# Kernel optimization log

Measured on AMD Instinct MI355X. Metric: run time of the kernel, lower is better.

The kernel has to match this reference:

```python
import jax, jax.numpy as jnp
import numpy as np

CHANNELS = 1024
T_LEN = 16384
WINDOW = 16
W_MIN, W_MAX = -1.0, 3.0
BETA = 0.95       # snn.Leaky(beta=0.95)
THRESHOLD = 1.0   # snn.Leaky(threshold=1)


def setup_inputs() -> dict:
    key = jax.random.key(0)
    inp = jax.random.normal(key, (CHANNELS, T_LEN), dtype=jnp.float32)
    return {"inp": inp}


def reference(inp):
    C, T = inp.shape
    pad = WINDOW // 2
    inp_padded = jnp.pad(inp, ((0, 0), (pad, pad)))  # [C, T + WINDOW]
    n_steps = T - WINDOW

    def step(carry, t):
        w, mem = carry
        # B: sliding window [C, WINDOW] starting at column t of padded input
        B = jax.lax.dynamic_slice(inp_padded, (0, t), (C, WINDOW))
        # mean(B @ B.T, axis=1) == B @ mean(B, axis=0)  -- avoids [C, C] intermediate
        B_ram = B @ jnp.mean(B, axis=0)
        w = jnp.clip(0.5 * w + 0.5 * B_ram, W_MIN, W_MAX)
        x = B[:, 0]  # == inp_padded[:, t]
        # snntorch Leaky, reset_mechanism='subtract':
        # reset from incoming mem, then mem = beta*mem + input - reset*thr, spk = mem > thr
        reset = (mem > THRESHOLD).astype(inp.dtype)
        mem = BETA * mem + w * x - reset * THRESHOLD
        spk = (mem > THRESHOLD).astype(inp.dtype)
        return (w, mem), spk

    w0 = jnp.ones((C,), dtype=inp.dtype)
    mem0 = jnp.zeros((C,), dtype=inp.dtype)
    _, spks = jax.lax.scan(step, (w0, mem0), jnp.arange(n_steps))  # spks: [n_steps, C]
    # out = deepcopy(inp); out[:, t] = spk for t < T - WINDOW
    out = inp.at[:, :n_steps].set(spks.T)
    return out
```

## Files before the change

### kernel.cpp

```cpp
#include <hip/hip_runtime.h>

#define C_CH   1024
#define T_DIM  16384
#define NSTEPS (T_DIM - 16)
#define PAD    8
#define TP     (T_DIM + 16)
#define CHUNK  256
#define NCHUNK 64
#define WARM   256

#define WS_CM_OFFSET (8u * T_DIM * sizeof(double))

__global__ void colsum_partial(const float* __restrict__ inp, double* __restrict__ part) {
    int col4 = (blockIdx.x * 256 + threadIdx.x) * 4;
    int rc   = blockIdx.y;
    const float* p = inp + (size_t)rc * 128 * T_DIM + col4;
    double ax = 0.0, ay = 0.0, az = 0.0, aw = 0.0;
    #pragma unroll 4
    for (int r = 0; r < 128; ++r) {
        float4 v = *(const float4*)(p + (size_t)r * T_DIM);
        ax += (double)v.x; ay += (double)v.y; az += (double)v.z; aw += (double)v.w;
    }
    double* q = part + (size_t)rc * T_DIM + col4;
    q[0] = ax; q[1] = ay; q[2] = az; q[3] = aw;
}

__global__ void colmean_tail(const double* __restrict__ part, const float* __restrict__ inp,
                             float* __restrict__ cm, float* __restrict__ out) {
    int i = blockIdx.x * 256 + threadIdx.x;
    if (i < TP) {
        float v = 0.0f;
        if (i >= PAD && i < T_DIM + PAD) {
            int col = i - PAD;
            double t = 0.0;
            #pragma unroll
            for (int r = 0; r < 8; ++r) t += part[(size_t)r * T_DIM + col];
            v = (float)(t * (1.0 / 1024.0));
        }
        cm[i] = v;
    }
    if (i < C_CH * 16) {
        int c = i >> 4, j = i & 15;
        size_t idx = (size_t)c * T_DIM + NSTEPS + j;
        out[idx] = inp[idx];
    }
}

__global__ __launch_bounds__(64) void scan_kernel(const float* __restrict__ inp,
                                                  const float* __restrict__ cm,
                                                  float* __restrict__ out) {
    const int k  = blockIdx.x;
    const int c  = blockIdx.y * 64 + threadIdx.x;
    const int t0 = k * CHUNK;
    const int tend = min(t0 + CHUNK, NSTEPS);
    const int tw = (k == 0) ? 0 : t0 - WARM;

    const float* row  = inp + (size_t)c * T_DIM;
    float*       orow = out + (size_t)c * T_DIM;

    float xs[16], ms[16];
    float win = 0.0f;
    #pragma unroll
    for (int j = 0; j < 16; ++j) {
        int s = tw + j;
        float x = (s >= PAD) ? row[s - PAD] : 0.0f;
        float m = cm[s];
        xs[j] = x; ms[j] = m;
        win = fmaf(x, m, win);
    }

    float w = 1.0f, mem = 0.0f;

    float4 a0 = *(const float4*)(row + tw + 8);
    float4 a1 = *(const float4*)(row + tw + 12);
    float4 a2 = *(const float4*)(row + tw + 16);
    float4 a3 = *(const float4*)(row + tw + 20);
    float4 b0 = *(const float4*)(cm + tw + 16);
    float4 b1 = *(const float4*)(cm + tw + 20);
    float4 b2 = *(const float4*)(cm + tw + 24);
    float4 b3 = *(const float4*)(cm + tw + 28);

    for (int t = tw; t < tend; t += 16) {
        float xn[16] = {a0.x,a0.y,a0.z,a0.w, a1.x,a1.y,a1.z,a1.w,
                        a2.x,a2.y,a2.z,a2.w, a3.x,a3.y,a3.z,a3.w};
        float mn[16] = {b0.x,b0.y,b0.z,b0.w, b1.x,b1.y,b1.z,b1.w,
                        b2.x,b2.y,b2.z,b2.w, b3.x,b3.y,b3.z,b3.w};

        int ts = (t + 16 < tend) ? (t + 16) : t;
        a0 = *(const float4*)(row + ts + 8);
        a1 = *(const float4*)(row + ts + 12);
        a2 = *(const float4*)(row + ts + 16);
        a3 = *(const float4*)(row + ts + 20);
        b0 = *(const float4*)(cm + ts + 16);
        b1 = *(const float4*)(cm + ts + 20);
        b2 = *(const float4*)(cm + ts + 24);
        b3 = *(const float4*)(cm + ts + 28);

        float spk[16];
        #pragma unroll
        for (int j = 0; j < 16; ++j) {
            w = fminf(fmaxf(fmaf(0.5f, w, 0.5f * win), -1.0f), 3.0f);
            float x = xs[j];
            float r = (mem > 1.0f) ? 1.0f : 0.0f;
            mem = fmaf(0.95f, mem, fmaf(w, x, -r));
            spk[j] = (mem > 1.0f) ? 1.0f : 0.0f;
            win = fmaf(xn[j], mn[j], fmaf(-x, ms[j], win));
            xs[j] = xn[j]; ms[j] = mn[j];
        }

        if (t >= t0) {
            *(float4*)(orow + t)      = make_float4(spk[0],  spk[1],  spk[2],  spk[3]);
            *(float4*)(orow + t + 4)  = make_float4(spk[4],  spk[5],  spk[6],  spk[7]);
            *(float4*)(orow + t + 8)  = make_float4(spk[8],  spk[9],  spk[10], spk[11]);
            *(float4*)(orow + t + 12) = make_float4(spk[12], spk[13], spk[14], spk[15]);
        }
    }
}

extern "C" void kernel_launch(void* const* d_in, const int* in_sizes, int n_in,
                              void* d_out, int out_size, void* d_ws, size_t ws_size,
                              hipStream_t stream) {
    const float* inp = (const float*)d_in[0];
    float* out = (float*)d_out;
    double* part = (double*)d_ws;
    float* cm = (float*)((char*)d_ws + WS_CM_OFFSET);

    colsum_partial<<<dim3(T_DIM / 1024, 8), 256, 0, stream>>>(inp, part);
    colmean_tail<<<dim3(65), 256, 0, stream>>>(part, inp, cm, out);
    scan_kernel<<<dim3(NCHUNK, C_CH / 64), 64, 0, stream>>>(inp, cm, out);
}
```

Measured before the change: 158.5 us.

## Stage scan input tiles via async global-to-LDS loads with swizzle and double buffering

The scan kernel now loads 64x64 input tiles cooperatively into double-buffered, XOR-swizzled shared memory using global_load_lds. This replaces per-thread strided row loads, which were uncoalesced across channels, and paces them with explicit vmcnt waits. It also remaps the block index to interleave chunks, writes spikes with nontemporal stores, and reshapes colsum_partial to 64-thread blocks with deeper unrolling. The cost is added complexity, hand-written waitcnt assumptions that could break ordering, and LDS use that may reduce occupancy.

```diff
diff --git a/kernel.cpp b/kernel.cpp
--- a/kernel.cpp
+++ b/kernel.cpp
@@ -8,15 +8,19 @@
 #define CHUNK  256
 #define NCHUNK 64
 #define WARM   256
+#define TILE   64
+
+typedef float vf4 __attribute__((ext_vector_type(4)));
 
 #define WS_CM_OFFSET (8u * T_DIM * sizeof(double))
 
-__global__ void colsum_partial(const float* __restrict__ inp, double* __restrict__ part) {
-    int col4 = (blockIdx.x * 256 + threadIdx.x) * 4;
+__global__ __launch_bounds__(64) void colsum_partial(const float* __restrict__ inp,
+                                                     double* __restrict__ part) {
+    int col4 = (blockIdx.x * 64 + threadIdx.x) * 4;
     int rc   = blockIdx.y;
     const float* p = inp + (size_t)rc * 128 * T_DIM + col4;
     double ax = 0.0, ay = 0.0, az = 0.0, aw = 0.0;
-    #pragma unroll 4
+    #pragma unroll 16
     for (int r = 0; r < 128; ++r) {
         float4 v = *(const float4*)(p + (size_t)r * T_DIM);
         ax += (double)v.x; ay += (double)v.y; az += (double)v.z; aw += (double)v.w;
@@ -46,55 +50,107 @@
     }
 }
 
+__device__ __forceinline__ void stage_tile(const float* __restrict__ inp, int ch0,
+                                           int col0, float* dst, int lane) {
+    const int sub = lane >> 4;
+    const int ci  = lane & 15;
+    #pragma unroll
+    for (int ii = 0; ii < 16; ++ii) {
+        int r   = 4 * ii + sub;
+        int q   = ci ^ (r & 7);
+        int col = col0 + q * 4;
+        col = min(max(col, 0), T_DIM - 4);
+        const float* src = inp + (size_t)(ch0 + r) * T_DIM + col;
+        __builtin_amdgcn_global_load_lds(
+            (const __attribute__((address_space(1))) void*)src,
+            (__attribute__((address_space(3))) void*)(dst + ii * 256),
+            16, 0, 0);
+    }
+}
+
 __global__ __launch_bounds__(64) void scan_kernel(const float* __restrict__ inp,
                                                   const float* __restrict__ cm,
                                                   float* __restrict__ out) {
-    const int k  = blockIdx.x;
-    const int c  = blockIdx.y * 64 + threadIdx.x;
-    const int t0 = k * CHUNK;
+    __shared__ float lds[2][64][TILE];
+
+    const int id   = blockIdx.x;
+    const int k    = ((id & 7) << 3) | ((id >> 3) & 7);
+    const int ygrp = id >> 6;
+    const int lane = threadIdx.x;
+    const int ch0  = ygrp * 64;
+    const int c    = ch0 + lane;
+    const int sw   = lane & 7;
+
+    const int t0   = k * CHUNK;
     const int tend = min(t0 + CHUNK, NSTEPS);
-    const int tw = (k == 0) ? 0 : t0 - WARM;
+    const int tw   = (k == 0) ? 0 : t0 - WARM;
+    const int base = tw - PAD;
+    const int span = tend - tw + 16;
+    const int ntiles = (span + TILE - 1) / TILE;
 
-    const float* row  = inp + (size_t)c * T_DIM;
-    float*       orow = out + (size_t)c * T_DIM;
+    float* orow = out + (size_t)c * T_DIM;
+
+    stage_tile(inp, ch0, base,        &lds[0][0][0], lane);
+    stage_tile(inp, ch0, base + TILE, &lds[1][0][0], lane);
+    asm volatile("s_waitcnt vmcnt(16)" ::: "memory");
 
     float xs[16], ms[16];
+    {
+        const float4* lrow0 = (const float4*)&lds[0][lane][0];
+        float4 i0 = lrow0[0 ^ sw];
+        float4 i1 = lrow0[1 ^ sw];
+        float4 i2 = lrow0[2 ^ sw];
+        float4 i3 = lrow0[3 ^ sw];
+        float tmp[16] = {i0.x,i0.y,i0.z,i0.w, i1.x,i1.y,i1.z,i1.w,
+                         i2.x,i2.y,i2.z,i2.w, i3.x,i3.y,i3.z,i3.w};
+        float4 m0 = *(const float4*)(cm + tw);
+        float4 m1 = *(const float4*)(cm + tw + 4);
+        float4 m2 = *(const float4*)(cm + tw + 8);
+        float4 m3 = *(const float4*)(cm + tw + 12);
+        float mt[16] = {m0.x,m0.y,m0.z,m0.w, m1.x,m1.y,m1.z,m1.w,
+                        m2.x,m2.y,m2.z,m2.w, m3.x,m3.y,m3.z,m3.w};
+        #pragma unroll
+        for (int j = 0; j < 16; ++j) {
+            xs[j] = (base + j < 0) ? 0.0f : tmp[j];
+            ms[j] = mt[j];
+        }
+    }
     float win = 0.0f;
     #pragma unroll
-    for (int j = 0; j < 16; ++j) {
-        int s = tw + j;
-        float x = (s >= PAD) ? row[s - PAD] : 0.0f;
-        float m = cm[s];
-        xs[j] = x; ms[j] = m;
-        win = fmaf(x, m, win);
-    }
+    for (int j = 0; j < 16; ++j) win = fmaf(xs[j], ms[j], win);
 
     float w = 1.0f, mem = 0.0f;
 
-    float4 a0 = *(const float4*)(row + tw + 8);
-    float4 a1 = *(const float4*)(row + tw + 12);
-    float4 a2 = *(const float4*)(row + tw + 16);
-    float4 a3 = *(const float4*)(row + tw + 20);
-    float4 b0 = *(const float4*)(cm + tw + 16);
-    float4 b1 = *(const float4*)(cm + tw + 20);
-    float4 b2 = *(const float4*)(cm + tw + 24);
-    float4 b3 = *(const float4*)(cm + tw + 28);
+    const int niter = (tend - tw) >> 4;
+    for (int i = 0; i < niter; ++i) {
+        const int t   = tw + (i << 4);
+        const int nxt = i + 1;
 
-    for (int t = tw; t < tend; t += 16) {
+        if ((nxt & 3) == 0) {
+            const int tn = nxt >> 2;
+            if (tn + 1 < ntiles) {
+                stage_tile(inp, ch0, base + (tn + 1) * TILE, &lds[(tn + 1) & 1][0][0], lane);
+                asm volatile("s_waitcnt vmcnt(16)" ::: "memory");
+            } else {
+                asm volatile("s_waitcnt vmcnt(0)" ::: "memory");
+            }
+        }
+
+        const float4* lrow = (const float4*)&lds[(nxt >> 2) & 1][lane][0];
+        const int qk = (nxt & 3) * 4;
+        float4 a0 = lrow[(qk + 0) ^ sw];
+        float4 a1 = lrow[(qk + 1) ^ sw];
+        float4 a2 = lrow[(qk + 2) ^ sw];
+        float4 a3 = lrow[(qk + 3) ^ sw];
+        float4 b0 = *(const float4*)(cm + t + 16);
+        float4 b1 = *(const float4*)(cm + t + 20);
+        float4 b2 = *(const float4*)(cm + t + 24);
+        float4 b3 = *(const float4*)(cm + t + 28);
+
         float xn[16] = {a0.x,a0.y,a0.z,a0.w, a1.x,a1.y,a1.z,a1.w,
                         a2.x,a2.y,a2.z,a2.w, a3.x,a3.y,a3.z,a3.w};
         float mn[16] = {b0.x,b0.y,b0.z,b0.w, b1.x,b1.y,b1.z,b1.w,
                         b2.x,b2.y,b2.z,b2.w, b3.x,b3.y,b3.z,b3.w};
-
-        int ts = (t + 16 < tend) ? (t + 16) : t;
-        a0 = *(const float4*)(row + ts + 8);
-        a1 = *(const float4*)(row + ts + 12);
-        a2 = *(const float4*)(row + ts + 16);
-        a3 = *(const float4*)(row + ts + 20);
-        b0 = *(const float4*)(cm + ts + 16);
-        b1 = *(const float4*)(cm + ts + 20);
-        b2 = *(const float4*)(cm + ts + 24);
-        b3 = *(const float4*)(cm + ts + 28);
 
         float spk[16];
         #pragma unroll
@@ -109,10 +165,14 @@
         }
 
         if (t >= t0) {
-            *(float4*)(orow + t)      = make_float4(spk[0],  spk[1],  spk[2],  spk[3]);
-            *(float4*)(orow + t + 4)  = make_float4(spk[4],  spk[5],  spk[6],  spk[7]);
-            *(float4*)(orow + t + 8)  = make_float4(spk[8],  spk[9],  spk[10], spk[11]);
-            *(float4*)(orow + t + 12) = make_float4(spk[12], spk[13], spk[14], spk[15]);
+            vf4 s0 = {spk[0],  spk[1],  spk[2],  spk[3]};
+            vf4 s1 = {spk[4],  spk[5],  spk[6],  spk[7]};
+            vf4 s2 = {spk[8],  spk[9],  spk[10], spk[11]};
+            vf4 s3 = {spk[12], spk[13], spk[14], spk[15]};
+            __builtin_nontemporal_store(s0, (vf4*)(orow + t));
+            __builtin_nontemporal_store(s1, (vf4*)(orow + t + 4));
+            __builtin_nontemporal_store(s2, (vf4*)(orow + t + 8));
+            __builtin_nontemporal_store(s3, (vf4*)(orow + t + 12));
         }
     }
 }
@@ -125,7 +185,7 @@
     double* part = (double*)d_ws;
     float* cm = (float*)((char*)d_ws + WS_CM_OFFSET);
 
-    colsum_partial<<<dim3(T_DIM / 1024, 8), 256, 0, stream>>>(inp, part);
+    colsum_partial<<<dim3(64, 8), 64, 0, stream>>>(inp, part);
     colmean_tail<<<dim3(65), 256, 0, stream>>>(part, inp, cm, out);
-    scan_kernel<<<dim3(NCHUNK, C_CH / 64), 64, 0, stream>>>(inp, cm, out);
+    scan_kernel<<<dim3(NCHUNK * (C_CH / 64)), 64, 0, stream>>>(inp, cm, out);
 }
```

New measurement: 255.5 us. 1.61x slower.

## Scan one channel per block with row staged in LDS and bitmask-coalesced output

Applied to the files above, without the earlier changes.

The scan kernel now gives each 64-lane block a single channel. The whole row is loaded into LDS through swizzled global_load_lds, and each lane handles a 256-step segment after warming up over the previous segment. Spikes are packed into bitmasks, exchanged through shared memory and written back as coalesced float4 stores, instead of each thread writing strided rows. The column-sum kernel also changes to 64-thread blocks with a deeper unroll. The block now uses about 64KB of LDS, which limits occupancy. The warmup still duplicates work, now at a fixed 256 steps per segment.

```diff
diff --git a/kernel.cpp b/kernel.cpp
--- a/kernel.cpp
+++ b/kernel.cpp
@@ -1,22 +1,22 @@
 #include <hip/hip_runtime.h>
+#include <stdint.h>
 
 #define C_CH   1024
 #define T_DIM  16384
 #define NSTEPS (T_DIM - 16)
 #define PAD    8
 #define TP     (T_DIM + 16)
-#define CHUNK  256
-#define NCHUNK 64
-#define WARM   256
+#define SEG    256
 
 #define WS_CM_OFFSET (8u * T_DIM * sizeof(double))
 
-__global__ void colsum_partial(const float* __restrict__ inp, double* __restrict__ part) {
-    int col4 = (blockIdx.x * 256 + threadIdx.x) * 4;
+__global__ __launch_bounds__(64) void colsum_partial(const float* __restrict__ inp,
+                                                     double* __restrict__ part) {
+    int col4 = (blockIdx.x * 64 + threadIdx.x) * 4;
     int rc   = blockIdx.y;
     const float* p = inp + (size_t)rc * 128 * T_DIM + col4;
     double ax = 0.0, ay = 0.0, az = 0.0, aw = 0.0;
-    #pragma unroll 4
+    #pragma unroll 32
     for (int r = 0; r < 128; ++r) {
         float4 v = *(const float4*)(p + (size_t)r * T_DIM);
         ax += (double)v.x; ay += (double)v.y; az += (double)v.z; aw += (double)v.w;
@@ -46,74 +46,130 @@
     }
 }
 
+__device__ __forceinline__ float4 swz_ld(const float* base, int b) {
+    int a = (b & ~1023) | ((((b >> 4) & 63) ^ ((b >> 10) & 7)) << 4);
+    return *(const float4*)((const char*)base + a);
+}
+
 __global__ __launch_bounds__(64) void scan_kernel(const float* __restrict__ inp,
                                                   const float* __restrict__ cm,
                                                   float* __restrict__ out) {
-    const int k  = blockIdx.x;
-    const int c  = blockIdx.y * 64 + threadIdx.x;
-    const int t0 = k * CHUNK;
-    const int tend = min(t0 + CHUNK, NSTEPS);
-    const int tw = (k == 0) ? 0 : t0 - WARM;
+    __shared__ float    rowl[T_DIM + 8];
+    __shared__ uint32_t bm[64][8];
 
-    const float* row  = inp + (size_t)c * T_DIM;
-    float*       orow = out + (size_t)c * T_DIM;
+    const int ch   = blockIdx.x;
+    const int lane = threadIdx.x;
+    const float* row  = inp + (size_t)ch * T_DIM;
+    float*       orow = out + (size_t)ch * T_DIM;
+
+    #pragma unroll
+    for (int i = 0; i < 64; ++i) {
+        const float* src = row + i * SEG + ((lane ^ (i & 7)) << 2);
+        __builtin_amdgcn_global_load_lds(
+            (const __attribute__((address_space(1))) void*)src,
+            (__attribute__((address_space(3))) void*)(rowl + i * SEG),
+            16, 0, 0);
+    }
+    if (lane < 2) {
+        *(float4*)(rowl + T_DIM + lane * 4) = make_float4(0.f, 0.f, 0.f, 0.f);
+    }
+    asm volatile("s_waitcnt vmcnt(0)" ::: "memory");
+    __builtin_amdgcn_sched_barrier(0);
+
+    const int sW = (lane == 0) ? 0 : (lane - 1) * SEG;
+    const int sM = lane * SEG;
 
     float xs[16], ms[16];
+    {
+        const float4* cp = (const float4*)(cm + sW);
+        float4 m0 = cp[0], m1 = cp[1], m2 = cp[2], m3 = cp[3];
+        float mt[16] = {m0.x,m0.y,m0.z,m0.w, m1.x,m1.y,m1.z,m1.w,
+                        m2.x,m2.y,m2.z,m2.w, m3.x,m3.y,m3.z,m3.w};
+        #pragma unroll
+        for (int j = 0; j < 16; ++j) ms[j] = mt[j];
+
+        if (sW == 0) {
+            float4 x2 = swz_ld(rowl, 0);
+            float4 x3 = swz_ld(rowl, 16);
+            float xt[8] = {x2.x,x2.y,x2.z,x2.w, x3.x,x3.y,x3.z,x3.w};
+            #pragma unroll
+            for (int j = 0; j < 8; ++j) { xs[j] = 0.0f; xs[j + 8] = xt[j]; }
+        } else {
+            const int b = sW * 4 - 32;
+            float4 x0 = swz_ld(rowl, b),      x1 = swz_ld(rowl, b + 16),
+                   x2 = swz_ld(rowl, b + 32), x3 = swz_ld(rowl, b + 48);
+            float xt[16] = {x0.x,x0.y,x0.z,x0.w, x1.x,x1.y,x1.z,x1.w,
+                            x2.x,x2.y,x2.z,x2.w, x3.x,x3.y,x3.z,x3.w};
+            #pragma unroll
+            for (int j = 0; j < 16; ++j) xs[j] = xt[j];
+        }
+    }
     float win = 0.0f;
     #pragma unroll
-    for (int j = 0; j < 16; ++j) {
-        int s = tw + j;
-        float x = (s >= PAD) ? row[s - PAD] : 0.0f;
-        float m = cm[s];
-        xs[j] = x; ms[j] = m;
-        win = fmaf(x, m, win);
+    for (int j = 0; j < 16; ++j) win = fmaf(xs[j], ms[j], win);
+
+    float w = 1.0f, mem = 0.0f, spf = 0.0f;
+
+    for (int it = 0; it < 16; ++it) {
+        if (lane != 0) {
+            const int b = sW * 4 + it * 64 + 32;
+            float4 a0 = swz_ld(rowl, b),      a1 = swz_ld(rowl, b + 16),
+                   a2 = swz_ld(rowl, b + 32), a3 = swz_ld(rowl, b + 48);
+            const float4* cp = (const float4*)(cm + sW + it * 16 + 16);
+            float4 b0 = cp[0], b1 = cp[1], b2 = cp[2], b3 = cp[3];
+            float xn[16] = {a0.x,a0.y,a0.z,a0.w, a1.x,a1.y,a1.z,a1.w,
+                            a2.x,a2.y,a2.z,a2.w, a3.x,a3.y,a3.z,a3.w};
+            float mn[16] = {b0.x,b0.y,b0.z,b0.w, b1.x,b1.y,b1.z,b1.w,
+                            b2.x,b2.y,b2.z,b2.w, b3.x,b3.y,b3.z,b3.w};
+            #pragma unroll
+            for (int j = 0; j < 16; ++j) {
+                w = fminf(fmaxf(fmaf(0.5f, w, 0.5f * win), -1.0f), 3.0f);
+                float x = xs[j];
+                mem = fmaf(0.95f, mem, fmaf(w, x, -spf));
+                spf = (mem > 1.0f) ? 1.0f : 0.0f;
+                win = fmaf(xn[j], mn[j], fmaf(-x, ms[j], win));
+                xs[j] = xn[j]; ms[j] = mn[j];
+            }
+        }
     }
 
-    float w = 1.0f, mem = 0.0f;
-
-    float4 a0 = *(const float4*)(row + tw + 8);
-    float4 a1 = *(const float4*)(row + tw + 12);
-    float4 a2 = *(const float4*)(row + tw + 16);
-    float4 a3 = *(const float4*)(row + tw + 20);
-    float4 b0 = *(const float4*)(cm + tw + 16);
-    float4 b1 = *(const float4*)(cm + tw + 20);
-    float4 b2 = *(const float4*)(cm + tw + 24);
-    float4 b3 = *(const float4*)(cm + tw + 28);
-
-    for (int t = tw; t < tend; t += 16) {
+    uint32_t sb[8] = {0, 0, 0, 0, 0, 0, 0, 0};
+    #pragma unroll
+    for (int q = 0; q < 16; ++q) {
+        const int b = sM * 4 + q * 64 + 32;
+        float4 a0 = swz_ld(rowl, b),      a1 = swz_ld(rowl, b + 16),
+               a2 = swz_ld(rowl, b + 32), a3 = swz_ld(rowl, b + 48);
+        const float4* cp = (const float4*)(cm + sM + q * 16 + 16);
+        float4 b0 = cp[0], b1 = cp[1], b2 = cp[2], b3 = cp[3];
         float xn[16] = {a0.x,a0.y,a0.z,a0.w, a1.x,a1.y,a1.z,a1.w,
                         a2.x,a2.y,a2.z,a2.w, a3.x,a3.y,a3.z,a3.w};
         float mn[16] = {b0.x,b0.y,b0.z,b0.w, b1.x,b1.y,b1.z,b1.w,
                         b2.x,b2.y,b2.z,b2.w, b3.x,b3.y,b3.z,b3.w};
-
-        int ts = (t + 16 < tend) ? (t + 16) : t;
-        a0 = *(const float4*)(row + ts + 8);
-        a1 = *(const float4*)(row + ts + 12);
-        a2 = *(const float4*)(row + ts + 16);
-        a3 = *(const float4*)(row + ts + 20);
-        b0 = *(const float4*)(cm + ts + 16);
-        b1 = *(const float4*)(cm + ts + 20);
-        b2 = *(const float4*)(cm + ts + 24);
-        b3 = *(const float4*)(cm + ts + 28);
-
-        float spk[16];
+        uint32_t m16 = 0;
         #pragma unroll
         for (int j = 0; j < 16; ++j) {
             w = fminf(fmaxf(fmaf(0.5f, w, 0.5f * win), -1.0f), 3.0f);
             float x = xs[j];
-            float r = (mem > 1.0f) ? 1.0f : 0.0f;
-            mem = fmaf(0.95f, mem, fmaf(w, x, -r));
-            spk[j] = (mem > 1.0f) ? 1.0f : 0.0f;
+            mem = fmaf(0.95f, mem, fmaf(w, x, -spf));
+            bool sp = (mem > 1.0f);
+            spf = sp ? 1.0f : 0.0f;
+            m16 |= sp ? (1u << j) : 0u;
             win = fmaf(xn[j], mn[j], fmaf(-x, ms[j], win));
             xs[j] = xn[j]; ms[j] = mn[j];
         }
+        sb[q >> 1] |= m16 << ((q & 1) * 16);
+    }
 
-        if (t >= t0) {
-            *(float4*)(orow + t)      = make_float4(spk[0],  spk[1],  spk[2],  spk[3]);
-            *(float4*)(orow + t + 4)  = make_float4(spk[4],  spk[5],  spk[6],  spk[7]);
-            *(float4*)(orow + t + 8)  = make_float4(spk[8],  spk[9],  spk[10], spk[11]);
-            *(float4*)(orow + t + 12) = make_float4(spk[12], spk[13], spk[14], spk[15]);
-        }
+    *(uint4*)&bm[lane][0] = make_uint4(sb[0], sb[1], sb[2], sb[3]);
+    *(uint4*)&bm[lane][4] = make_uint4(sb[4], sb[5], sb[6], sb[7]);
+    #pragma unroll 8
+    for (int seg = 0; seg < 64; ++seg) {
+        uint32_t word = bm[seg][lane >> 3];
+        uint32_t bits = (word >> ((lane & 7) * 4)) & 0xFu;
+        float4 v = make_float4((bits & 1u) ? 1.f : 0.f, (bits & 2u) ? 1.f : 0.f,
+                               (bits & 4u) ? 1.f : 0.f, (bits & 8u) ? 1.f : 0.f);
+        if (seg < 63 || lane < 60)
+            *(float4*)(orow + seg * SEG + lane * 4) = v;
     }
 }
 
@@ -125,7 +181,7 @@
     double* part = (double*)d_ws;
     float* cm = (float*)((char*)d_ws + WS_CM_OFFSET);
 
-    colsum_partial<<<dim3(T_DIM / 1024, 8), 256, 0, stream>>>(inp, part);
+    colsum_partial<<<dim3(64, 8), 64, 0, stream>>>(inp, part);
     colmean_tail<<<dim3(65), 256, 0, stream>>>(part, inp, cm, out);
-    scan_kernel<<<dim3(NCHUNK, C_CH / 64), 64, 0, stream>>>(inp, cm, out);
+    scan_kernel<<<dim3(C_CH), 64, 0, stream>>>(inp, cm, out);
 }
```

After: 154.3 us. 1.03x faster.
